# Optimization experiments

Hardware: AMD Instinct MI355X
Metric: run time of the kernel (lower is better)

## Reference

```python
import jax, jax.numpy as jnp
import numpy as np

EMBED = 1024
HEADS = 16
HEAD_DIM = EMBED // HEADS


def setup_inputs() -> dict:
    key = jax.random.key(0)
    ks = jax.random.split(key, 12)
    B, S, E = 2, 2048, EMBED
    scale = 1.0 / np.sqrt(E)
    inp = {
        "query": jax.random.normal(ks[0], (B, S, E), jnp.float32),
        "key": jax.random.normal(ks[1], (B, S, E), jnp.float32),
        "value": jax.random.normal(ks[2], (B, S, E), jnp.float32),
        "Wq": jax.random.normal(ks[3], (E, E), jnp.float32) * scale,
        "bq": jax.random.normal(ks[4], (E,), jnp.float32) * 0.01,
        "Wk": jax.random.normal(ks[5], (E, E), jnp.float32) * scale,
        "bk": jax.random.normal(ks[6], (E,), jnp.float32) * 0.01,
        "Wv": jax.random.normal(ks[7], (E, E), jnp.float32) * scale,
        "bv": jax.random.normal(ks[8], (E,), jnp.float32) * 0.01,
        "Wo": jax.random.normal(ks[9], (E, E), jnp.float32) * scale,
        "bo": jax.random.normal(ks[10], (E,), jnp.float32) * 0.01,
    }
    return inp


def reference(query, key, value, Wq, bq, Wk, bk, Wv, bv, Wo, bo):
    B, Sq, E = query.shape
    Sk = key.shape[1]
    H, D = HEADS, HEAD_DIM
    # QKV projections (torch Linear: x @ W.T + b)
    q = (query @ Wq.T + bq).reshape(B, Sq, H, D)
    k = (key @ Wk.T + bk).reshape(B, Sk, H, D)
    v = (value @ Wv.T + bv).reshape(B, Sk, H, D)
    # energy: [B, H, Sq, Sk]; note scale = 1/sqrt(embed_size), not head_dim
    energy = jnp.einsum("bqhd,bkhd->bhqk", q, k)
    scale = jnp.asarray(E, energy.dtype) ** 0.5
    attn = jax.nn.softmax(energy / scale, axis=-1)
    out = jnp.einsum("bhqk,bkhd->bqhd", attn, v).reshape(B, Sq, E)
    # fc_out (dropout is identity at eval)
    return out @ Wo.T + bo
```

## Files before the change

kernel.cpp:

```cpp
#include <hip/hip_runtime.h>
#include <hip/hip_bf16.h>

typedef __hip_bfloat16 bf16;
typedef short frag8 __attribute__((ext_vector_type(8)));
typedef _Float16 half4 __attribute__((ext_vector_type(4)));
typedef float f32x4 __attribute__((ext_vector_type(4)));

typedef __attribute__((address_space(3))) void lds_void;
typedef __attribute__((address_space(1))) const void gbl_void;

__device__ __forceinline__ void gld16(const void* g, void* l) {
  __builtin_amdgcn_global_load_lds((gbl_void*)g, (lds_void*)l, 16, 0, 0);
}

__device__ __forceinline__ unsigned short f2bf(float f) {
  union { float f; unsigned u; } x; x.f = f;
  unsigned r = x.u + 0x7FFFu + ((x.u >> 16) & 1u);
  return (unsigned short)(r >> 16);
}

#define QSCALE 0.0450842200278f
#define MFIX 4.0f

struct CvtArgs {
  const float4* src[7];
  ushort4* dst[7];
  int n4[7];
};
__global__ __launch_bounds__(256) void cvt_all(CvtArgs a) {
  const int t = blockIdx.y;
  const int i = blockIdx.x * 256 + threadIdx.x;
  if (i >= a.n4[t]) return;
  float4 v = a.src[t][i];
  ushort4 o;
  o.x = f2bf(v.x); o.y = f2bf(v.y); o.z = f2bf(v.z); o.w = f2bf(v.w);
  a.dst[t][i] = o;
}

template<int MODE>
__global__ __launch_bounds__(256)
void gemm_bt(const bf16* __restrict__ A0, const bf16* __restrict__ A1, const bf16* __restrict__ A2,
             const bf16* __restrict__ W0, const bf16* __restrict__ W1, const bf16* __restrict__ W2,
             const float* __restrict__ b0, const float* __restrict__ b1, const float* __restrict__ b2,
             void* __restrict__ o0, void* __restrict__ o1, void* __restrict__ o2) {
  constexpr int NK = 1024;
  constexpr int BN = (MODE == 1) ? 128 : 64;
  __shared__ __align__(16) bf16 As[2][128 * 32];
  __shared__ __align__(16) bf16 Bs[2][BN * 32];
  const int tid = threadIdx.x;
  const int wave = tid >> 6, lane = tid & 63, quad = lane >> 4, l16 = lane & 15;
  const int wm = wave >> 1, wn = wave & 1;
  const int bn = blockIdx.x, bm = blockIdx.y;

  const bf16* A = A0; const bf16* W = W0; const float* bias = b0; void* out = o0;
  int z = 0;
  if constexpr (MODE == 1) {
    z = blockIdx.z;
    if (z == 1) { A = A1; W = W1; bias = b1; out = o1; }
    else if (z == 2) { A = A2; W = W2; bias = b2; out = o2; }
  }

  const bf16* Ab = A + (size_t)bm * 128 * NK;
  const bf16* Wb = W + (size_t)bn * BN * NK;
  const int c0_ = tid & 3, r0_ = tid >> 2;
  const int rc = (quad ^ (l16 & 3)) << 3;

  auto stageA = [&](int k0, int buf) {
    #pragma unroll
    for (int is = 0; is < 2; ++is) {
      const int c = tid + is * 256;
      const int r = r0_ + is * 64;
      const int gc = (c0_ ^ (r & 3)) << 3;
      gld16(Ab + (size_t)r * NK + k0 + gc, (void*)(&As[buf][(size_t)c * 8]));
    }
  };
  auto stageW = [&](int k0, int buf) {
    if constexpr (MODE == 1) {
      #pragma unroll
      for (int is = 0; is < 2; ++is) {
        const int c = tid + is * 256;
        const int r = r0_ + is * 64;
        const int gc = (c0_ ^ (r & 3)) << 3;
        gld16(Wb + (size_t)r * NK + k0 + gc, (void*)(&Bs[buf][(size_t)c * 8]));
      }
    } else {
      const int r = r0_;
      const int gc = (c0_ ^ (r & 3)) << 3;
      gld16(Wb + (size_t)r * NK + k0 + gc, (void*)(&Bs[buf][(size_t)tid * 8]));
    }
  };

  if constexpr (MODE == 1) {
    f32x4 acc[4][4];
    #pragma unroll
    for (int i = 0; i < 4; ++i)
      #pragma unroll
      for (int j = 0; j < 4; ++j)
        acc[i][j] = (f32x4){0.f, 0.f, 0.f, 0.f};

    stageA(0, 0); stageW(0, 0);
    #pragma unroll 2
    for (int kt = 0; kt < 32; ++kt) {
      __syncthreads();
      if (kt < 31) { stageA((kt + 1) * 32, (kt + 1) & 1); stageW((kt + 1) * 32, (kt + 1) & 1); }
      const bf16* as_ = As[kt & 1];
      const bf16* bs_ = Bs[kt & 1];
      frag8 af[4], bfr[4];
      #pragma unroll
      for (int i = 0; i < 4; ++i)
        af[i] = *(const frag8*)&as_[(wm * 64 + i * 16 + l16) * 32 + rc];
      #pragma unroll
      for (int j = 0; j < 4; ++j)
        bfr[j] = *(const frag8*)&bs_[(wn * 64 + j * 16 + l16) * 32 + rc];
      #pragma unroll
      for (int i = 0; i < 4; ++i)
        #pragma unroll
        for (int j = 0; j < 4; ++j)
          acc[i][j] = __builtin_amdgcn_mfma_f32_16x16x32_bf16(af[i], bfr[j], acc[i][j], 0, 0, 0);
    }

    #pragma unroll
    for (int j = 0; j < 4; ++j) {
      const int col = bn * 128 + wn * 64 + j * 16 + l16;
      const float bv = bias[col];
      #pragma unroll
      for (int i = 0; i < 4; ++i) {
        #pragma unroll
        for (int r = 0; r < 4; ++r) {
          const int row = bm * 128 + wm * 64 + i * 16 + quad * 4 + r;
          float v = acc[i][j][r] + bv;
          const int b = row >> 11, s = row & 2047;
          const int hh = col >> 6, d = col & 63;
          const size_t bh = (size_t)(b * 16 + hh);
          if (z == 0) {
            v *= QSCALE;
            ((bf16*)out)[(bh * 2048 + s) * 64 + d] = __float2bfloat16(v);
          } else if (z == 1) {
            const int rr = s & 127;
            const size_t addr = bh * 131072 + (size_t)(s >> 7) * 8192 + (size_t)rr * 64
                              + (size_t)(((d >> 3) ^ (rr & 7)) << 3) + (d & 7);
            ((bf16*)out)[addr] = __float2bfloat16(v);
          } else {
            const int kvl = s & 127;
            const size_t addr = bh * 131072 + (size_t)(s >> 7) * 8192 + (size_t)d * 128
                              + (size_t)((((kvl >> 2) ^ (d & 15)) << 2)) + (kvl & 3);
            ((_Float16*)out)[addr] = (_Float16)v;
          }
        }
      }
    }
  } else {
    f32x4 acc[4][2];
    #pragma unroll
    for (int i = 0; i < 4; ++i)
      #pragma unroll
      for (int j = 0; j < 2; ++j)
        acc[i][j] = (f32x4){0.f, 0.f, 0.f, 0.f};

    stageA(0, 0); stageW(0, 0);
    #pragma unroll 2
    for (int kt = 0; kt < 32; ++kt) {
      __syncthreads();
      if (kt < 31) { stageA((kt + 1) * 32, (kt + 1) & 1); stageW((kt + 1) * 32, (kt + 1) & 1); }
      const bf16* as_ = As[kt & 1];
      const bf16* bs_ = Bs[kt & 1];
      frag8 af[4], bfr[2];
      #pragma unroll
      for (int i = 0; i < 4; ++i)
        af[i] = *(const frag8*)&as_[(wm * 64 + i * 16 + l16) * 32 + rc];
      #pragma unroll
      for (int j = 0; j < 2; ++j)
        bfr[j] = *(const frag8*)&bs_[(wn * 32 + j * 16 + l16) * 32 + rc];
      #pragma unroll
      for (int i = 0; i < 4; ++i)
        #pragma unroll
        for (int j = 0; j < 2; ++j)
          acc[i][j] = __builtin_amdgcn_mfma_f32_16x16x32_bf16(af[i], bfr[j], acc[i][j], 0, 0, 0);
    }

    #pragma unroll
    for (int j = 0; j < 2; ++j) {
      const int col = bn * 64 + wn * 32 + j * 16 + l16;
      const float bv = bias[col];
      #pragma unroll
      for (int i = 0; i < 4; ++i) {
        #pragma unroll
        for (int r = 0; r < 4; ++r) {
          const int row = bm * 128 + wm * 64 + i * 16 + quad * 4 + r;
          ((float*)out)[(size_t)row * 1024 + col] = acc[i][j][r] + bv;
        }
      }
    }
  }
}

__global__ __launch_bounds__(256)
void flash_attn(const bf16* __restrict__ Q, const bf16* __restrict__ K,
                const _Float16* __restrict__ Vt, bf16* __restrict__ ctx) {
  __shared__ __align__(16) bf16 Ks[2][128 * 64];
  __shared__ __align__(16) _Float16 Vs[2][64 * 128];
  const int tid = threadIdx.x;
  const int wave = tid >> 6, lane = tid & 63, quad = lane >> 4, l16 = lane & 15;
  const int bh = blockIdx.x, b = bh >> 4, h = bh & 15;
  const int q0 = blockIdx.y * 128 + wave * 32;
  const bf16* Qb = Q + (size_t)bh * 2048 * 64;
  const bf16* Kb = K + (size_t)bh * 131072;
  const _Float16* Vb = Vt + (size_t)bh * 131072;

  frag8 qf[2][2];
  #pragma unroll
  for (int qt = 0; qt < 2; ++qt)
    #pragma unroll
    for (int ks = 0; ks < 2; ++ks)
      qf[qt][ks] = *(const frag8*)(Qb + (size_t)(q0 + qt * 16 + l16) * 64 + ks * 32 + quad * 8);

  f32x4 rsv[2];
  f32x4 o[2][4];
  #pragma unroll
  for (int qt = 0; qt < 2; ++qt) {
    rsv[qt] = (f32x4){0.f, 0.f, 0.f, 0.f};
    #pragma unroll
    for (int dt = 0; dt < 4; ++dt)
      o[qt][dt] = (f32x4){0.f, 0.f, 0.f, 0.f};
  }

  const int xk = l16 & 7;

  auto stage = [&](int kt, int buf) {
    #pragma unroll
    for (int is = 0; is < 4; ++is) {
      const int c = tid + is * 256;
      gld16(Kb + (size_t)kt * 8192 + (size_t)c * 8, (void*)(&Ks[buf][(size_t)c * 8]));
      gld16(Vb + (size_t)kt * 8192 + (size_t)c * 8, (void*)(&Vs[buf][(size_t)c * 8]));
    }
  };

  stage(0, 0);
  #pragma unroll 2
  for (int kt = 0; kt < 16; ++kt) {
    __syncthreads();
    if (kt < 15) stage(kt + 1, (kt + 1) & 1);
    const bf16* ks_ = Ks[kt & 1];
    const _Float16* vs_ = Vs[kt & 1];

    f32x4 s[2][8];
    #pragma unroll
    for (int qt = 0; qt < 2; ++qt)
      #pragma unroll
      for (int jt = 0; jt < 8; ++jt)
        s[qt][jt] = (f32x4){-MFIX, -MFIX, -MFIX, -MFIX};
    #pragma unroll
    for (int ks = 0; ks < 2; ++ks) {
      frag8 kf[8];
      #pragma unroll
      for (int jt = 0; jt < 8; ++jt)
        kf[jt] = *(const frag8*)&ks_[(jt * 16 + l16) * 64 + (((ks * 4 + quad) ^ xk) << 3)];
      #pragma unroll
      for (int qt = 0; qt < 2; ++qt)
        #pragma unroll
        for (int jt = 0; jt < 8; ++jt)
          s[qt][jt] = __builtin_amdgcn_mfma_f32_16x16x32_bf16(kf[jt], qf[qt][ks], s[qt][jt], 0, 0, 0);
    }

    half4 pf[2][8];
    #pragma unroll
    for (int qt = 0; qt < 2; ++qt) {
      #pragma unroll
      for (int jt = 0; jt < 8; ++jt) {
        f32x4 p4;
        #pragma unroll
        for (int r = 0; r < 4; ++r)
          p4[r] = __builtin_amdgcn_exp2f(s[qt][jt][r]);
        rsv[qt] += p4;
        #pragma unroll
        for (int r = 0; r < 4; ++r)
          pf[qt][jt][r] = (_Float16)p4[r];
      }
    }

    #pragma unroll
    for (int jt = 0; jt < 8; ++jt) {
      half4 vf[4];
      #pragma unroll
      for (int dt = 0; dt < 4; ++dt)
        vf[dt] = *(const half4*)&vs_[(dt * 16 + l16) * 128 + (((jt * 4 + quad) ^ l16) << 2)];
      #pragma unroll
      for (int qt = 0; qt < 2; ++qt)
        #pragma unroll
        for (int dt = 0; dt < 4; ++dt)
          o[qt][dt] = __builtin_amdgcn_mfma_f32_16x16x16f16(vf[dt], pf[qt][jt], o[qt][dt], 0, 0, 0);
    }
  }

  #pragma unroll
  for (int qt = 0; qt < 2; ++qt) {
    float l = rsv[qt][0] + rsv[qt][1] + rsv[qt][2] + rsv[qt][3];
    l += __shfl_xor(l, 16, 64);
    l += __shfl_xor(l, 32, 64);
    const float inv = __builtin_amdgcn_rcpf(l);
    const int q = q0 + qt * 16 + l16;
    #pragma unroll
    for (int dt = 0; dt < 4; ++dt) {
      ushort4 w;
      w.x = f2bf(o[qt][dt][0] * inv);
      w.y = f2bf(o[qt][dt][1] * inv);
      w.z = f2bf(o[qt][dt][2] * inv);
      w.w = f2bf(o[qt][dt][3] * inv);
      const int d = dt * 16 + quad * 4;
      *(uint2*)&ctx[((size_t)(b * 2048 + q)) * 1024 + h * 64 + d] = *(uint2*)&w;
    }
  }
}

extern "C" void kernel_launch(void* const* d_in, const int* in_sizes, int n_in,
                              void* d_out, int out_size, void* d_ws, size_t ws_size,
                              hipStream_t stream) {
  const float* q_in = (const float*)d_in[0];
  const float* k_in = (const float*)d_in[1];
  const float* v_in = (const float*)d_in[2];
  const float* Wq = (const float*)d_in[3];
  const float* bq = (const float*)d_in[4];
  const float* Wk = (const float*)d_in[5];
  const float* bk = (const float*)d_in[6];
  const float* Wv = (const float*)d_in[7];
  const float* bv = (const float*)d_in[8];
  const float* Wo = (const float*)d_in[9];
  const float* bo = (const float*)d_in[10];

  char* ws = (char*)d_ws;
  const size_t MB = 1024 * 1024;
  bf16* Xq  = (bf16*)(ws + 0 * MB);
  bf16* Xk  = (bf16*)(ws + 8 * MB);
  bf16* Xv  = (bf16*)(ws + 16 * MB);
  bf16* Wqb = (bf16*)(ws + 24 * MB);
  bf16* Wkb = (bf16*)(ws + 26 * MB);
  bf16* Wvb = (bf16*)(ws + 28 * MB);
  bf16* Wob = (bf16*)(ws + 30 * MB);
  bf16* Qw  = (bf16*)(ws + 32 * MB);
  bf16* Kw  = (bf16*)(ws + 40 * MB);
  _Float16* Vtw = (_Float16*)(ws + 48 * MB);
  bf16* Ctx = (bf16*)(ws + 56 * MB);

  {
    CvtArgs a;
    a.src[0] = (const float4*)q_in; a.dst[0] = (ushort4*)Xq;  a.n4[0] = 4194304 / 4;
    a.src[1] = (const float4*)k_in; a.dst[1] = (ushort4*)Xk;  a.n4[1] = 4194304 / 4;
    a.src[2] = (const float4*)v_in; a.dst[2] = (ushort4*)Xv;  a.n4[2] = 4194304 / 4;
    a.src[3] = (const float4*)Wq;   a.dst[3] = (ushort4*)Wqb; a.n4[3] = 1048576 / 4;
    a.src[4] = (const float4*)Wk;   a.dst[4] = (ushort4*)Wkb; a.n4[4] = 1048576 / 4;
    a.src[5] = (const float4*)Wv;   a.dst[5] = (ushort4*)Wvb; a.n4[5] = 1048576 / 4;
    a.src[6] = (const float4*)Wo;   a.dst[6] = (ushort4*)Wob; a.n4[6] = 1048576 / 4;
    cvt_all<<<dim3(4096, 7), 256, 0, stream>>>(a);
  }

  gemm_bt<1><<<dim3(8, 32, 3), 256, 0, stream>>>(Xq, Xk, Xv, Wqb, Wkb, Wvb,
                                                 bq, bk, bv, Qw, Kw, (bf16*)Vtw);
  flash_attn<<<dim3(32, 16), 256, 0, stream>>>(Qw, Kw, Vtw, Ctx);
  gemm_bt<0><<<dim3(16, 32), 256, 0, stream>>>(Ctx, nullptr, nullptr, Wob, nullptr, nullptr,
                                               bo, nullptr, nullptr, d_out, nullptr, nullptr);
}
```

Before: 236.8 us.

## Replace QKV projection GEMM with 256x256-tile, 8-wave pipelined kernel

Adds a new QKV projection kernel that uses 256x256 output tiles, 512 threads and a K-step of 64, split into two 32-wide halves. It uses double-buffered direct global-to-LDS loads with a swizzled layout, and interleaves the next tile's loads with MFMA phases under s_setprio and fine-grained waitcnt. The aim is more operand reuse per LDS byte and better overlap of memory with compute than the 128x128 gemm_bt version. In exchange it holds a large accumulator per thread (128 floats) and uses 128KB of LDS. The grid drops to 192 blocks, which may underfill the 256 CUs.

```diff
diff --git a/kernel.cpp b/kernel.cpp
--- a/kernel.cpp
+++ b/kernel.cpp
@@ -35,6 +35,164 @@
   ushort4 o;
   o.x = f2bf(v.x); o.y = f2bf(v.y); o.z = f2bf(v.z); o.w = f2bf(v.w);
   a.dst[t][i] = o;
+}
+
+template<int J0>
+__device__ __forceinline__ void mfma16(f32x4 (&acc)[8][4], const frag8 (&af)[8], const frag8 (&bf2)[2]) {
+  __builtin_amdgcn_s_setprio(1);
+  #pragma unroll
+  for (int i = 0; i < 8; ++i) {
+    #pragma unroll
+    for (int j = 0; j < 2; ++j)
+      acc[i][J0 + j] = __builtin_amdgcn_mfma_f32_16x16x32_bf16(af[i], bf2[j], acc[i][J0 + j], 0, 0, 0);
+  }
+  __builtin_amdgcn_s_setprio(0);
+}
+
+__global__ __launch_bounds__(512, 2)
+void gemm_qkv256(const bf16* __restrict__ A0, const bf16* __restrict__ A1, const bf16* __restrict__ A2,
+                 const bf16* __restrict__ W0, const bf16* __restrict__ W1, const bf16* __restrict__ W2,
+                 const float* __restrict__ b0, const float* __restrict__ b1, const float* __restrict__ b2,
+                 void* __restrict__ o0, void* __restrict__ o1, void* __restrict__ o2) {
+  __shared__ __align__(16) bf16 As[2][16384];
+  __shared__ __align__(16) bf16 Bs[2][16384];
+  const int tid = threadIdx.x;
+  const int wave = tid >> 6, lane = tid & 63, quad = lane >> 4, l16 = lane & 15;
+  const int wm = wave >> 2, wn = wave & 3;
+  const int bn = blockIdx.x, bm = blockIdx.y, z = blockIdx.z;
+
+  const bf16* A = A0; const bf16* W = W0; const float* bias = b0; void* out = o0;
+  if (z == 1) { A = A1; W = W1; bias = b1; out = o1; }
+  else if (z == 2) { A = A2; W = W2; bias = b2; out = o2; }
+
+  const bf16* Ab = A + (size_t)bm * 256 * 1024;
+  const bf16* Wb = W + (size_t)bn * 256 * 1024;
+  const int c0_ = tid & 3, r0_ = tid >> 2;
+  const int gcp = ((c0_ ^ ((r0_ >> 1) & 3)) << 3);
+  const int rc2 = (quad ^ ((l16 >> 1) & 3)) << 3;
+
+  auto stage = [&](const bf16* src, int kt, int kh, bf16* dst) {
+    #pragma unroll
+    for (int is = 0; is < 2; ++is) {
+      const int r = r0_ + is * 128;
+      gld16(src + (size_t)r * 1024 + kt * 64 + kh * 32 + gcp,
+            (void*)(dst + (is * 512 + tid) * 8));
+    }
+  };
+  auto ldsA = [&](const bf16* ah, frag8 (&af)[8]) {
+    #pragma unroll
+    for (int i = 0; i < 8; ++i)
+      af[i] = *(const frag8*)&ah[(wm * 128 + i * 16 + l16) * 32 + rc2];
+  };
+  auto ldsB2 = [&](const bf16* bh, int j0, frag8 (&bf2)[2]) {
+    #pragma unroll
+    for (int j = 0; j < 2; ++j)
+      bf2[j] = *(const frag8*)&bh[(wn * 64 + (j0 + j) * 16 + l16) * 32 + rc2];
+  };
+
+  f32x4 acc[8][4];
+  #pragma unroll
+  for (int i = 0; i < 8; ++i)
+    #pragma unroll
+    for (int j = 0; j < 4; ++j)
+      acc[i][j] = (f32x4){0.f, 0.f, 0.f, 0.f};
+
+  stage(Ab, 0, 0, &As[0][0]);
+  stage(Wb, 0, 0, &Bs[0][0]);
+  stage(Ab, 0, 1, &As[0][8192]);
+  stage(Wb, 0, 1, &Bs[0][8192]);
+  asm volatile("s_waitcnt vmcnt(0)" ::: "memory");
+  __builtin_amdgcn_s_barrier();
+
+  #pragma unroll 2
+  for (int t = 0; t < 15; ++t) {
+    const int buf = t & 1, nb = buf ^ 1;
+    const bf16* a0 = &As[buf][0];    const bf16* a1 = &As[buf][8192];
+    const bf16* b0 = &Bs[buf][0];    const bf16* b1 = &Bs[buf][8192];
+    frag8 af[8], bf2[2];
+
+    ldsA(a0, af); ldsB2(b0, 0, bf2);
+    stage(Ab, t + 1, 0, &As[nb][0]);
+    __builtin_amdgcn_s_barrier();
+    asm volatile("s_waitcnt lgkmcnt(0)" ::: "memory");
+    mfma16<0>(acc, af, bf2);
+    __builtin_amdgcn_s_barrier();
+
+    ldsB2(b0, 2, bf2);
+    stage(Wb, t + 1, 0, &Bs[nb][0]);
+    asm volatile("s_waitcnt vmcnt(4)" ::: "memory");
+    __builtin_amdgcn_s_barrier();
+    asm volatile("s_waitcnt lgkmcnt(0)" ::: "memory");
+    mfma16<2>(acc, af, bf2);
+    __builtin_amdgcn_s_barrier();
+
+    ldsA(a1, af); ldsB2(b1, 0, bf2);
+    stage(Ab, t + 1, 1, &As[nb][8192]);
+    __builtin_amdgcn_s_barrier();
+    asm volatile("s_waitcnt lgkmcnt(0)" ::: "memory");
+    mfma16<0>(acc, af, bf2);
+    __builtin_amdgcn_s_barrier();
+
+    ldsB2(b1, 2, bf2);
+    stage(Wb, t + 1, 1, &Bs[nb][8192]);
+    asm volatile("s_waitcnt vmcnt(4)" ::: "memory");
+    __builtin_amdgcn_s_barrier();
+    asm volatile("s_waitcnt lgkmcnt(0)" ::: "memory");
+    mfma16<2>(acc, af, bf2);
+    __builtin_amdgcn_s_barrier();
+  }
+
+  {
+    const bf16* a0 = &As[1][0];    const bf16* a1 = &As[1][8192];
+    const bf16* b0 = &Bs[1][0];    const bf16* b1 = &Bs[1][8192];
+    frag8 af[8], bf2[2];
+    ldsA(a0, af); ldsB2(b0, 0, bf2);
+    __builtin_amdgcn_s_barrier();
+    asm volatile("s_waitcnt lgkmcnt(0)" ::: "memory");
+    mfma16<0>(acc, af, bf2);
+    ldsB2(b0, 2, bf2);
+    asm volatile("s_waitcnt vmcnt(0)" ::: "memory");
+    __builtin_amdgcn_s_barrier();
+    asm volatile("s_waitcnt lgkmcnt(0)" ::: "memory");
+    mfma16<2>(acc, af, bf2);
+    ldsA(a1, af); ldsB2(b1, 0, bf2);
+    asm volatile("s_waitcnt lgkmcnt(0)" ::: "memory");
+    mfma16<0>(acc, af, bf2);
+    ldsB2(b1, 2, bf2);
+    asm volatile("s_waitcnt lgkmcnt(0)" ::: "memory");
+    mfma16<2>(acc, af, bf2);
+  }
+
+  #pragma unroll
+  for (int j = 0; j < 4; ++j) {
+    const int col = bn * 256 + wn * 64 + j * 16 + l16;
+    const float bv = bias[col];
+    #pragma unroll
+    for (int i = 0; i < 8; ++i) {
+      #pragma unroll
+      for (int r = 0; r < 4; ++r) {
+        const int row = bm * 256 + wm * 128 + i * 16 + quad * 4 + r;
+        float v = acc[i][j][r] + bv;
+        const int b = row >> 11, s = row & 2047;
+        const int hh = col >> 6, d = col & 63;
+        const size_t bh = (size_t)(b * 16 + hh);
+        if (z == 0) {
+          v *= QSCALE;
+          ((bf16*)out)[(bh * 2048 + s) * 64 + d] = __float2bfloat16(v);
+        } else if (z == 1) {
+          const int rr = s & 127;
+          const size_t addr = bh * 131072 + (size_t)(s >> 7) * 8192 + (size_t)rr * 64
+                            + (size_t)(((d >> 3) ^ (rr & 7)) << 3) + (d & 7);
+          ((bf16*)out)[addr] = __float2bfloat16(v);
+        } else {
+          const int kvl = s & 127;
+          const size_t addr = bh * 131072 + (size_t)(s >> 7) * 8192 + (size_t)d * 128
+                            + (size_t)((((kvl >> 2) ^ (d & 15)) << 2)) + (kvl & 3);
+          ((_Float16*)out)[addr] = (_Float16)v;
+        }
+      }
+    }
+  }
 }
 
 template<int MODE>
@@ -353,8 +511,8 @@
     cvt_all<<<dim3(4096, 7), 256, 0, stream>>>(a);
   }
 
-  gemm_bt<1><<<dim3(8, 32, 3), 256, 0, stream>>>(Xq, Xk, Xv, Wqb, Wkb, Wvb,
-                                                 bq, bk, bv, Qw, Kw, (bf16*)Vtw);
+  gemm_qkv256<<<dim3(4, 16, 3), 512, 0, stream>>>(Xq, Xk, Xv, Wqb, Wkb, Wvb,
+                                                  bq, bk, bv, Qw, Kw, (bf16*)Vtw);
   flash_attn<<<dim3(32, 16), 256, 0, stream>>>(Qw, Kw, Vtw, Ctx);
   gemm_bt<0><<<dim3(16, 32), 256, 0, stream>>>(Ctx, nullptr, nullptr, Wob, nullptr, nullptr,
                                                bo, nullptr, nullptr, d_out, nullptr, nullptr);
```

Result: faster. 227.0 us (-4.1%).
